# Kernel optimization log

Hardware: AMD Instinct MI355X
Metric: run time of the kernel (lower is better)

Reference implementation:

```python
import jax, jax.numpy as jnp
import numpy as np
import math

D_MODEL = 512
NUM_HEADS = 8
HEAD_DIM = D_MODEL // NUM_HEADS
B, S = 4, 2048


def setup_inputs() -> dict:
    key = jax.random.key(0)
    ks = jax.random.split(key, 11)
    scale = 1.0 / math.sqrt(D_MODEL)
    inp = {
        "Q": jax.random.normal(ks[0], (B, S, D_MODEL), jnp.float32),
        "K": jax.random.normal(ks[1], (B, S, D_MODEL), jnp.float32),
        "V": jax.random.normal(ks[2], (B, S, D_MODEL), jnp.float32),
        # causal mask, broadcast over batch and heads: [1,1,S,S]
        "mask": jnp.tril(jnp.ones((S, S), dtype=bool))[None, None],
        "w_q": jax.random.normal(ks[3], (D_MODEL, D_MODEL), jnp.float32) * scale,
        "b_q": jnp.zeros((D_MODEL,), jnp.float32),
        "w_k": jax.random.normal(ks[4], (D_MODEL, D_MODEL), jnp.float32) * scale,
        "b_k": jnp.zeros((D_MODEL,), jnp.float32),
        "w_v": jax.random.normal(ks[5], (D_MODEL, D_MODEL), jnp.float32) * scale,
        "b_v": jnp.zeros((D_MODEL,), jnp.float32),
        "w_o": jax.random.normal(ks[6], (D_MODEL, D_MODEL), jnp.float32) * scale,
        "b_o": jnp.zeros((D_MODEL,), jnp.float32),
    }
    return inp


def _split_heads(x):
    b, s, _ = x.shape
    return x.reshape(b, s, NUM_HEADS, HEAD_DIM).transpose(0, 2, 1, 3)  # [B,H,S,Dh]


def reference(Q, K, V, mask, w_q, b_q, w_k, b_k, w_v, b_v, w_o, b_o):
    # Linear projections (torch Linear: x @ W.T + b)
    q = _split_heads(Q @ w_q.T + b_q)
    k = _split_heads(K @ w_k.T + b_k)
    v = _split_heads(V @ w_v.T + b_v)

    scores = jnp.einsum("bhqd,bhkd->bhqk", q, k) / math.sqrt(HEAD_DIM)
    scores = jnp.where(mask, scores, -jnp.inf)
    attention = jax.nn.softmax(scores, axis=-1)  # [B,H,S,S]
    ctx = jnp.einsum("bhqk,bhkd->bhqd", attention, v)

    b, h, s, dh = ctx.shape
    x = ctx.transpose(0, 2, 1, 3).reshape(b, s, D_MODEL)
    x = x @ w_o.T + b_o
    return (x, attention)
```

## Files before the change

kernel.cpp:

```cpp
#include <hip/hip_runtime.h>


#define BATCH 4
#define SEQ   2048
#define DM    512
#define NH    8
#define DH    64
#define ROWS  (BATCH*SEQ)
#define QT    (SEQ/64)

typedef unsigned short u16;
using bf8   = __attribute__((ext_vector_type(8))) short;
using f32x4 = __attribute__((ext_vector_type(4))) float;

__device__ __forceinline__ float b2f(u16 u) {
    union { unsigned int i; float f; } v; v.i = ((unsigned int)u) << 16; return v.f;
}
__device__ __forceinline__ u16 f2b(float f) {
    union { float fl; unsigned int i; } v; v.fl = f;
    return (u16)((v.i + 0x7FFFu + ((v.i >> 16) & 1u)) >> 16);
}

template<bool IN_BF16, bool OUT_BF16>
__global__ __launch_bounds__(256) void proj_mfma(
    const void* __restrict__ Xv, const float* __restrict__ W,
    const float* __restrict__ bias, void* __restrict__ Cv)
{
    __shared__ u16 Xs[128][40];
    __shared__ u16 Wsh[128][40];
    const int tid  = threadIdx.x;
    const int lane = tid & 63;
    const int w    = tid >> 6;
    const int wm = (w >> 1) * 64, wn = (w & 1) * 64;
    const int lc = lane & 15, lq = lane >> 4;
    const int row0 = blockIdx.y * 128;
    const int col0 = blockIdx.x * 128;

    const f32x4 fzero = {0.f, 0.f, 0.f, 0.f};
    f32x4 acc[4][4];
    #pragma unroll
    for (int mt = 0; mt < 4; ++mt)
        #pragma unroll
        for (int nt = 0; nt < 4; ++nt) acc[mt][nt] = fzero;

    for (int k0 = 0; k0 < DM; k0 += 32) {
        __syncthreads();
        if (IN_BF16) {
            const u16* Xg = (const u16*)Xv;
            const int r = tid >> 2, kc = (tid & 3) * 8;
            #pragma unroll
            for (int rr = 0; rr < 2; ++rr)
                *(bf8*)&Xs[r + rr*64][kc] =
                    *(const bf8*)(Xg + (size_t)(row0 + r + rr*64) * DM + k0 + kc);
        } else {
            const float* Xg = (const float*)Xv;
            const int r = tid >> 3, kc = (tid & 7) * 4;
            #pragma unroll
            for (int rr = 0; rr < 4; ++rr) {
                float4 vx = *(const float4*)(Xg + (size_t)(row0 + r + rr*32) * DM + k0 + kc);
                u16 t4[4] = { f2b(vx.x), f2b(vx.y), f2b(vx.z), f2b(vx.w) };
                *(uint2*)&Xs[r + rr*32][kc] = *(uint2*)t4;
            }
        }
        {
            const int r = tid >> 3, kc = (tid & 7) * 4;
            #pragma unroll
            for (int rr = 0; rr < 4; ++rr) {
                float4 vw = *(const float4*)(W + (size_t)(col0 + r + rr*32) * DM + k0 + kc);
                u16 t4[4] = { f2b(vw.x), f2b(vw.y), f2b(vw.z), f2b(vw.w) };
                *(uint2*)&Wsh[r + rr*32][kc] = *(uint2*)t4;
            }
        }
        __syncthreads();
        bf8 a[4], b[4];
        #pragma unroll
        for (int mt = 0; mt < 4; ++mt) a[mt] = *(const bf8*)&Xs[wm + mt*16 + lc][lq*8];
        #pragma unroll
        for (int nt = 0; nt < 4; ++nt) b[nt] = *(const bf8*)&Wsh[wn + nt*16 + lc][lq*8];
        #pragma unroll
        for (int mt = 0; mt < 4; ++mt)
            #pragma unroll
            for (int nt = 0; nt < 4; ++nt)
                acc[mt][nt] = __builtin_amdgcn_mfma_f32_16x16x32_bf16(a[mt], b[nt], acc[mt][nt], 0, 0, 0);
    }
    #pragma unroll
    for (int nt = 0; nt < 4; ++nt) {
        const int col = col0 + wn + nt*16 + lc;
        const float bv = bias[col];
        #pragma unroll
        for (int mt = 0; mt < 4; ++mt) {
            #pragma unroll
            for (int r = 0; r < 4; ++r) {
                const int row = row0 + wm + mt*16 + lq*4 + r;
                const float val = acc[mt][nt][r] + bv;
                if (OUT_BF16) ((u16*)Cv)[(size_t)row * DM + col] = f2b(val);
                else          ((float*)Cv)[(size_t)row * DM + col] = val;
            }
        }
    }
}

__global__ __launch_bounds__(256) void attn_ml(
    const u16* __restrict__ q, const u16* __restrict__ k,
    float* __restrict__ mrow, float* __restrict__ lrow)
{
    __shared__ u16 Qs[64][72];
    __shared__ u16 Ks[64][72];
    __shared__ float Ms[64][17];
    __shared__ float Ls[64][17];
    const int tid = threadIdx.x, lane = tid & 63, w = tid >> 6;
    const int lc = lane & 15, lq = lane >> 4;
    const int h = blockIdx.y, b = blockIdx.z;
    const size_t base = ((size_t)b * SEQ) * DM + h * DH;
    const int sr = tid >> 3, sc = (tid & 7) * 8;
    const f32x4 fzero = {0.f, 0.f, 0.f, 0.f};

    for (int qi = 0; qi < 2; ++qi) {
        const int qt = qi ? (QT - 1 - (int)blockIdx.x) : (int)blockIdx.x;
        __syncthreads();
        #pragma unroll
        for (int rr = 0; rr < 2; ++rr)
            *(bf8*)&Qs[sr + rr*32][sc] =
                *(const bf8*)(q + base + (size_t)(qt*64 + sr + rr*32) * DM + sc);

        float m_p[4], l_p[4];
        #pragma unroll
        for (int r = 0; r < 4; ++r) { m_p[r] = -1e30f; l_p[r] = 0.f; }

        for (int kt = 0; kt <= qt; ++kt) {
            __syncthreads();
            #pragma unroll
            for (int rr = 0; rr < 2; ++rr)
                *(bf8*)&Ks[sr + rr*32][sc] =
                    *(const bf8*)(k + base + (size_t)(kt*64 + sr + rr*32) * DM + sc);
            __syncthreads();
            f32x4 s[4];
            #pragma unroll
            for (int nt = 0; nt < 4; ++nt) s[nt] = fzero;
            #pragma unroll
            for (int ks = 0; ks < 2; ++ks) {
                bf8 a = *(const bf8*)&Qs[w*16 + lc][ks*32 + lq*8];
                #pragma unroll
                for (int nt = 0; nt < 4; ++nt) {
                    bf8 bb = *(const bf8*)&Ks[nt*16 + lc][ks*32 + lq*8];
                    s[nt] = __builtin_amdgcn_mfma_f32_16x16x32_bf16(a, bb, s[nt], 0, 0, 0);
                }
            }
            const bool diag = (kt == qt);
            #pragma unroll
            for (int r = 0; r < 4; ++r) {
                const int rowl = w*16 + lq*4 + r;
                float sv[4];
                #pragma unroll
                for (int nt = 0; nt < 4; ++nt) {
                    float x = s[nt][r] * 0.125f;
                    if (diag && (nt*16 + lc > rowl)) x = -1e30f;
                    sv[nt] = x;
                }
                const float tm = fmaxf(fmaxf(sv[0], sv[1]), fmaxf(sv[2], sv[3]));
                const float mnew = fmaxf(m_p[r], tm);
                float add = __expf(sv[0]-mnew) + __expf(sv[1]-mnew)
                          + __expf(sv[2]-mnew) + __expf(sv[3]-mnew);
                l_p[r] = l_p[r] * __expf(m_p[r] - mnew) + add;
                m_p[r] = mnew;
            }
        }
        #pragma unroll
        for (int r = 0; r < 4; ++r) {
            Ms[w*16 + lq*4 + r][lc] = m_p[r];
            Ls[w*16 + lq*4 + r][lc] = l_p[r];
        }
        __syncthreads();
        if (tid < 64) {
            float mf = -1e30f;
            #pragma unroll
            for (int t = 0; t < 16; ++t) mf = fmaxf(mf, Ms[tid][t]);
            float lf = 0.f;
            #pragma unroll
            for (int t = 0; t < 16; ++t) lf += Ls[tid][t] * __expf(Ms[tid][t] - mf);
            const size_t n = ((size_t)(b * NH + h)) * SEQ + qt*64 + tid;
            mrow[n] = mf;
            lrow[n] = lf;
        }
    }
}

__global__ __launch_bounds__(256) void attn_av(
    const u16* __restrict__ q, const u16* __restrict__ k, const u16* __restrict__ v,
    const float* __restrict__ mrow, const float* __restrict__ lrow,
    float* __restrict__ att, u16* __restrict__ ctx)
{
    __shared__ u16 Qs[64][72];
    __shared__ u16 Ks[64][72];
    __shared__ u16 Vt[64][72];
    __shared__ u16 Ps[64][72];
    __shared__ float Mv[64];
    __shared__ float Lv[64];
    const int tid = threadIdx.x, lane = tid & 63, w = tid >> 6;
    const int lc = lane & 15, lq = lane >> 4;
    const int h = blockIdx.y, b = blockIdx.z;
    const size_t base = ((size_t)b * SEQ) * DM + h * DH;
    const size_t attbase = ((size_t)(b * NH + h)) * SEQ * SEQ;
    const int sr = tid >> 3, sc = (tid & 7) * 8;
    const f32x4 fzero = {0.f, 0.f, 0.f, 0.f};

    for (int qi = 0; qi < 2; ++qi) {
        const int qt = qi ? (QT - 1 - (int)blockIdx.x) : (int)blockIdx.x;
        __syncthreads();
        #pragma unroll
        for (int rr = 0; rr < 2; ++rr)
            *(bf8*)&Qs[sr + rr*32][sc] =
                *(const bf8*)(q + base + (size_t)(qt*64 + sr + rr*32) * DM + sc);
        if (tid < 64) {
            const size_t n = ((size_t)(b * NH + h)) * SEQ + qt*64 + tid;
            Mv[tid] = mrow[n];
            Lv[tid] = 1.0f / lrow[n];
        }
        f32x4 oc[4];
        #pragma unroll
        for (int nt = 0; nt < 4; ++nt) oc[nt] = fzero;

        for (int kt = 0; kt <= qt; ++kt) {
            __syncthreads();
            #pragma unroll
            for (int rr = 0; rr < 2; ++rr)
                *(bf8*)&Ks[sr + rr*32][sc] =
                    *(const bf8*)(k + base + (size_t)(kt*64 + sr + rr*32) * DM + sc);
            {
                const int dv = tid & 63, jg = (tid >> 6) * 16;
                u16 tv[16];
                #pragma unroll
                for (int i = 0; i < 16; ++i)
                    tv[i] = v[base + (size_t)(kt*64 + jg + i) * DM + dv];
                *(bf8*)&Vt[dv][jg]     = *(bf8*)&tv[0];
                *(bf8*)&Vt[dv][jg + 8] = *(bf8*)&tv[8];
            }
            __syncthreads();
            f32x4 s[4];
            #pragma unroll
            for (int nt = 0; nt < 4; ++nt) s[nt] = fzero;
            #pragma unroll
            for (int ks = 0; ks < 2; ++ks) {
                bf8 a = *(const bf8*)&Qs[w*16 + lc][ks*32 + lq*8];
                #pragma unroll
                for (int nt = 0; nt < 4; ++nt) {
                    bf8 bb = *(const bf8*)&Ks[nt*16 + lc][ks*32 + lq*8];
                    s[nt] = __builtin_amdgcn_mfma_f32_16x16x32_bf16(a, bb, s[nt], 0, 0, 0);
                }
            }
            const bool diag = (kt == qt);
            #pragma unroll
            for (int nt = 0; nt < 4; ++nt) {
                #pragma unroll
                for (int r = 0; r < 4; ++r) {
                    const int rowl = w*16 + lq*4 + r;
                    const int coll = nt*16 + lc;
                    float p = 0.f;
                    if (!diag || coll <= rowl)
                        p = __expf(s[nt][r] * 0.125f - Mv[rowl]) * Lv[rowl];
                    att[attbase + (size_t)(qt*64 + rowl) * SEQ + kt*64 + coll] = p;
                    Ps[rowl][coll] = f2b(p);
                }
            }
            __syncthreads();
            #pragma unroll
            for (int ks = 0; ks < 2; ++ks) {
                bf8 a = *(const bf8*)&Ps[w*16 + lc][ks*32 + lq*8];
                #pragma unroll
                for (int nt = 0; nt < 4; ++nt) {
                    bf8 bb = *(const bf8*)&Vt[nt*16 + lc][ks*32 + lq*8];
                    oc[nt] = __builtin_amdgcn_mfma_f32_16x16x32_bf16(a, bb, oc[nt], 0, 0, 0);
                }
            }
        }
        #pragma unroll
        for (int nt = 0; nt < 4; ++nt) {
            #pragma unroll
            for (int r = 0; r < 4; ++r) {
                const int rowl = w*16 + lq*4 + r;
                ctx[((size_t)b * SEQ + qt*64 + rowl) * DM + h*DH + nt*16 + lc] = f2b(oc[nt][r]);
            }
        }
        {
            const int zr = tid >> 2, zc0 = (tid & 3) * 16;
            const float4 z = {0.f, 0.f, 0.f, 0.f};
            for (int ct = qt + 1; ct < QT; ++ct) {
                #pragma unroll
                for (int jj = 0; jj < 4; ++jj)
                    *(float4*)(att + attbase + (size_t)(qt*64 + zr) * SEQ + ct*64 + zc0 + jj*4) = z;
            }
        }
    }
}

extern "C" void kernel_launch(void* const* d_in, const int* in_sizes, int n_in,
                              void* d_out, int out_size, void* d_ws, size_t ws_size,
                              hipStream_t stream) {
    const float* Q   = (const float*)d_in[0];
    const float* K   = (const float*)d_in[1];
    const float* V   = (const float*)d_in[2];
    const float* w_q = (const float*)d_in[4];
    const float* b_q = (const float*)d_in[5];
    const float* w_k = (const float*)d_in[6];
    const float* b_k = (const float*)d_in[7];
    const float* w_v = (const float*)d_in[8];
    const float* b_v = (const float*)d_in[9];
    const float* w_o = (const float*)d_in[10];
    const float* b_o = (const float*)d_in[11];

    float* x_out   = (float*)d_out;
    float* att_out = x_out + (size_t)ROWS * DM;

    u16* qw = (u16*)d_ws;
    u16* kw = qw + (size_t)ROWS * DM;
    u16* vw = kw + (size_t)ROWS * DM;
    u16* cw = vw + (size_t)ROWS * DM;
    float* mr = (float*)(cw + (size_t)ROWS * DM);
    float* lr = mr + (size_t)BATCH * NH * SEQ;

    dim3 pgrid(DM/128, ROWS/128);
    proj_mfma<false, true><<<pgrid, 256, 0, stream>>>(Q, w_q, b_q, qw);
    proj_mfma<false, true><<<pgrid, 256, 0, stream>>>(K, w_k, b_k, kw);
    proj_mfma<false, true><<<pgrid, 256, 0, stream>>>(V, w_v, b_v, vw);

    dim3 agrid(QT/2, NH, BATCH);
    attn_ml<<<agrid, 256, 0, stream>>>(qw, kw, mr, lr);
    attn_av<<<agrid, 256, 0, stream>>>(qw, kw, vw, mr, lr, att_out, cw);

    proj_mfma<true, false><<<pgrid, 256, 0, stream>>>(cw, w_o, b_o, x_out);
}
```

Before: 879.1 us.

## Fuse softmax-stats and AV attention kernels with double-buffered K/V prefetch

The separate row max/sum kernel and the probability/AV kernel become one kernel. Each block computes the softmax statistics for its query tile in shared memory and then runs the P·V pass, so the mrow/lrow round-trip through global memory, the second Q load and one kernel launch all go away. Both K loops now double-buffer K (and V in the second pass) in shared memory, prefetching the next tile into registers while the current tile computes. This removes one barrier per iteration. The trade-off is more shared memory per block, which may lower occupancy.

Result: faster. 806.5 us (-8.3%).

```diff
diff --git a/kernel.cpp b/kernel.cpp
--- a/kernel.cpp
+++ b/kernel.cpp
@@ -100,19 +100,26 @@
     }
 }
 
-__global__ __launch_bounds__(256) void attn_ml(
-    const u16* __restrict__ q, const u16* __restrict__ k,
-    float* __restrict__ mrow, float* __restrict__ lrow)
+__global__ __launch_bounds__(256) void attn_fused(
+    const u16* __restrict__ q, const u16* __restrict__ k, const u16* __restrict__ v,
+    float* __restrict__ att, u16* __restrict__ ctx)
 {
     __shared__ u16 Qs[64][72];
-    __shared__ u16 Ks[64][72];
+    __shared__ u16 Ks[2][64][72];
+    __shared__ u16 Vt[2][64][72];
+    __shared__ u16 Ps[64][72];
     __shared__ float Ms[64][17];
     __shared__ float Ls[64][17];
+    __shared__ float Mv[64];
+    __shared__ float Lv[64];
+
     const int tid = threadIdx.x, lane = tid & 63, w = tid >> 6;
     const int lc = lane & 15, lq = lane >> 4;
     const int h = blockIdx.y, b = blockIdx.z;
     const size_t base = ((size_t)b * SEQ) * DM + h * DH;
+    const size_t attbase = ((size_t)(b * NH + h)) * SEQ * SEQ;
     const int sr = tid >> 3, sc = (tid & 7) * 8;
+    const int dv = tid & 63, jg = (tid >> 6) * 16;
     const f32x4 fzero = {0.f, 0.f, 0.f, 0.f};
 
     for (int qi = 0; qi < 2; ++qi) {
@@ -127,13 +134,22 @@
         #pragma unroll
         for (int r = 0; r < 4; ++r) { m_p[r] = -1e30f; l_p[r] = 0.f; }
 
+        bf8 kr[2];
+        #pragma unroll
+        for (int rr = 0; rr < 2; ++rr)
+            kr[rr] = *(const bf8*)(k + base + (size_t)(sr + rr*32) * DM + sc);
+        #pragma unroll
+        for (int rr = 0; rr < 2; ++rr)
+            *(bf8*)&Ks[0][sr + rr*32][sc] = kr[rr];
+
+        int cur = 0;
         for (int kt = 0; kt <= qt; ++kt) {
             __syncthreads();
-            #pragma unroll
-            for (int rr = 0; rr < 2; ++rr)
-                *(bf8*)&Ks[sr + rr*32][sc] =
-                    *(const bf8*)(k + base + (size_t)(kt*64 + sr + rr*32) * DM + sc);
-            __syncthreads();
+            if (kt < qt) {
+                #pragma unroll
+                for (int rr = 0; rr < 2; ++rr)
+                    kr[rr] = *(const bf8*)(k + base + (size_t)((kt+1)*64 + sr + rr*32) * DM + sc);
+            }
             f32x4 s[4];
             #pragma unroll
             for (int nt = 0; nt < 4; ++nt) s[nt] = fzero;
@@ -142,7 +158,7 @@
                 bf8 a = *(const bf8*)&Qs[w*16 + lc][ks*32 + lq*8];
                 #pragma unroll
                 for (int nt = 0; nt < 4; ++nt) {
-                    bf8 bb = *(const bf8*)&Ks[nt*16 + lc][ks*32 + lq*8];
+                    bf8 bb = *(const bf8*)&Ks[cur][nt*16 + lc][ks*32 + lq*8];
                     s[nt] = __builtin_amdgcn_mfma_f32_16x16x32_bf16(a, bb, s[nt], 0, 0, 0);
                 }
             }
@@ -164,12 +180,26 @@
                 l_p[r] = l_p[r] * __expf(m_p[r] - mnew) + add;
                 m_p[r] = mnew;
             }
-        }
+            if (kt < qt) {
+                #pragma unroll
+                for (int rr = 0; rr < 2; ++rr)
+                    *(bf8*)&Ks[cur^1][sr + rr*32][sc] = kr[rr];
+            }
+            cur ^= 1;
+        }
+
         #pragma unroll
         for (int r = 0; r < 4; ++r) {
             Ms[w*16 + lq*4 + r][lc] = m_p[r];
             Ls[w*16 + lq*4 + r][lc] = l_p[r];
         }
+        #pragma unroll
+        for (int rr = 0; rr < 2; ++rr)
+            kr[rr] = *(const bf8*)(k + base + (size_t)(sr + rr*32) * DM + sc);
+        u16 tv[16];
+        #pragma unroll
+        for (int i = 0; i < 16; ++i)
+            tv[i] = v[base + (size_t)(jg + i) * DM + dv];
         __syncthreads();
         if (tid < 64) {
             float mf = -1e30f;
@@ -178,64 +208,30 @@
             float lf = 0.f;
             #pragma unroll
             for (int t = 0; t < 16; ++t) lf += Ls[tid][t] * __expf(Ms[tid][t] - mf);
-            const size_t n = ((size_t)(b * NH + h)) * SEQ + qt*64 + tid;
-            mrow[n] = mf;
-            lrow[n] = lf;
-        }
-    }
-}
-
-__global__ __launch_bounds__(256) void attn_av(
-    const u16* __restrict__ q, const u16* __restrict__ k, const u16* __restrict__ v,
-    const float* __restrict__ mrow, const float* __restrict__ lrow,
-    float* __restrict__ att, u16* __restrict__ ctx)
-{
-    __shared__ u16 Qs[64][72];
-    __shared__ u16 Ks[64][72];
-    __shared__ u16 Vt[64][72];
-    __shared__ u16 Ps[64][72];
-    __shared__ float Mv[64];
-    __shared__ float Lv[64];
-    const int tid = threadIdx.x, lane = tid & 63, w = tid >> 6;
-    const int lc = lane & 15, lq = lane >> 4;
-    const int h = blockIdx.y, b = blockIdx.z;
-    const size_t base = ((size_t)b * SEQ) * DM + h * DH;
-    const size_t attbase = ((size_t)(b * NH + h)) * SEQ * SEQ;
-    const int sr = tid >> 3, sc = (tid & 7) * 8;
-    const f32x4 fzero = {0.f, 0.f, 0.f, 0.f};
-
-    for (int qi = 0; qi < 2; ++qi) {
-        const int qt = qi ? (QT - 1 - (int)blockIdx.x) : (int)blockIdx.x;
-        __syncthreads();
-        #pragma unroll
-        for (int rr = 0; rr < 2; ++rr)
-            *(bf8*)&Qs[sr + rr*32][sc] =
-                *(const bf8*)(q + base + (size_t)(qt*64 + sr + rr*32) * DM + sc);
-        if (tid < 64) {
-            const size_t n = ((size_t)(b * NH + h)) * SEQ + qt*64 + tid;
-            Mv[tid] = mrow[n];
-            Lv[tid] = 1.0f / lrow[n];
-        }
+            Mv[tid] = mf;
+            Lv[tid] = 1.0f / lf;
+        }
+        #pragma unroll
+        for (int rr = 0; rr < 2; ++rr)
+            *(bf8*)&Ks[0][sr + rr*32][sc] = kr[rr];
+        *(bf8*)&Vt[0][dv][jg]     = *(bf8*)&tv[0];
+        *(bf8*)&Vt[0][dv][jg + 8] = *(bf8*)&tv[8];
+
         f32x4 oc[4];
         #pragma unroll
         for (int nt = 0; nt < 4; ++nt) oc[nt] = fzero;
 
+        cur = 0;
         for (int kt = 0; kt <= qt; ++kt) {
             __syncthreads();
-            #pragma unroll
-            for (int rr = 0; rr < 2; ++rr)
-                *(bf8*)&Ks[sr + rr*32][sc] =
-                    *(const bf8*)(k + base + (size_t)(kt*64 + sr + rr*32) * DM + sc);
-            {
-                const int dv = tid & 63, jg = (tid >> 6) * 16;
-                u16 tv[16];
+            if (kt < qt) {
+                #pragma unroll
+                for (int rr = 0; rr < 2; ++rr)
+                    kr[rr] = *(const bf8*)(k + base + (size_t)((kt+1)*64 + sr + rr*32) * DM + sc);
                 #pragma unroll
                 for (int i = 0; i < 16; ++i)
-                    tv[i] = v[base + (size_t)(kt*64 + jg + i) * DM + dv];
-                *(bf8*)&Vt[dv][jg]     = *(bf8*)&tv[0];
-                *(bf8*)&Vt[dv][jg + 8] = *(bf8*)&tv[8];
-            }
-            __syncthreads();
+                    tv[i] = v[base + (size_t)((kt+1)*64 + jg + i) * DM + dv];
+            }
             f32x4 s[4];
             #pragma unroll
             for (int nt = 0; nt < 4; ++nt) s[nt] = fzero;
@@ -244,7 +240,7 @@
                 bf8 a = *(const bf8*)&Qs[w*16 + lc][ks*32 + lq*8];
                 #pragma unroll
                 for (int nt = 0; nt < 4; ++nt) {
-                    bf8 bb = *(const bf8*)&Ks[nt*16 + lc][ks*32 + lq*8];
+                    bf8 bb = *(const bf8*)&Ks[cur][nt*16 + lc][ks*32 + lq*8];
                     s[nt] = __builtin_amdgcn_mfma_f32_16x16x32_bf16(a, bb, s[nt], 0, 0, 0);
                 }
             }
@@ -262,16 +258,23 @@
                     Ps[rowl][coll] = f2b(p);
                 }
             }
-            __syncthreads();
             #pragma unroll
             for (int ks = 0; ks < 2; ++ks) {
                 bf8 a = *(const bf8*)&Ps[w*16 + lc][ks*32 + lq*8];
                 #pragma unroll
                 for (int nt = 0; nt < 4; ++nt) {
-                    bf8 bb = *(const bf8*)&Vt[nt*16 + lc][ks*32 + lq*8];
+                    bf8 bb = *(const bf8*)&Vt[cur][nt*16 + lc][ks*32 + lq*8];
                     oc[nt] = __builtin_amdgcn_mfma_f32_16x16x32_bf16(a, bb, oc[nt], 0, 0, 0);
                 }
             }
+            if (kt < qt) {
+                #pragma unroll
+                for (int rr = 0; rr < 2; ++rr)
+                    *(bf8*)&Ks[cur^1][sr + rr*32][sc] = kr[rr];
+                *(bf8*)&Vt[cur^1][dv][jg]     = *(bf8*)&tv[0];
+                *(bf8*)&Vt[cur^1][dv][jg + 8] = *(bf8*)&tv[8];
+            }
+            cur ^= 1;
         }
         #pragma unroll
         for (int nt = 0; nt < 4; ++nt) {
@@ -315,8 +318,6 @@
     u16* kw = qw + (size_t)ROWS * DM;
     u16* vw = kw + (size_t)ROWS * DM;
     u16* cw = vw + (size_t)ROWS * DM;
-    float* mr = (float*)(cw + (size_t)ROWS * DM);
-    float* lr = mr + (size_t)BATCH * NH * SEQ;
 
     dim3 pgrid(DM/128, ROWS/128);
     proj_mfma<false, true><<<pgrid, 256, 0, stream>>>(Q, w_q, b_q, qw);
@@ -324,8 +325,7 @@
     proj_mfma<false, true><<<pgrid, 256, 0, stream>>>(V, w_v, b_v, vw);
 
     dim3 agrid(QT/2, NH, BATCH);
-    attn_ml<<<agrid, 256, 0, stream>>>(qw, kw, mr, lr);
-    attn_av<<<agrid, 256, 0, stream>>>(qw, kw, vw, mr, lr, att_out, cw);
+    attn_fused<<<agrid, 256, 0, stream>>>(qw, kw, vw, att_out, cw);
 
     proj_mfma<true, false><<<pgrid, 256, 0, stream>>>(cw, w_o, b_o, x_out);
 }
```
